# Kernel optimization log

Measured on AMD Instinct MI355X. Metric: run time of the kernel, lower is better.

The kernel has to match this reference:

```python
import jax, jax.numpy as jnp
import numpy as np

B, L, D, H, MLP = 8, 1024, 768, 12, 3072
DH = D // H
EPS = 1e-5


def setup_inputs() -> dict:
    key = jax.random.key(0)
    ks = jax.random.split(key, 8)
    s = 0.02
    return {
        "x": jax.random.normal(ks[0], (B, L, D), dtype=jnp.float32),
        "ln1_g": jnp.ones((D,), jnp.float32),
        "ln1_b": jnp.zeros((D,), jnp.float32),
        "w_qkv": jax.random.normal(ks[1], (3 * D, D), dtype=jnp.float32) * s,
        "w_out": jax.random.normal(ks[2], (D, D), dtype=jnp.float32) * s,
        "b_out": jnp.zeros((D,), jnp.float32),
        "ln2_g": jnp.ones((D,), jnp.float32),
        "ln2_b": jnp.zeros((D,), jnp.float32),
        "w1": jax.random.normal(ks[3], (MLP, D), dtype=jnp.float32) * s,
        "b1": jnp.zeros((MLP,), jnp.float32),
        "w2": jax.random.normal(ks[4], (D, MLP), dtype=jnp.float32) * s,
        "b2": jnp.zeros((D,), jnp.float32),
    }


def _layernorm(x, g, b):
    mu = jnp.mean(x, axis=-1, keepdims=True)
    var = jnp.mean(jnp.square(x - mu), axis=-1, keepdims=True)
    return (x - mu) * jax.lax.rsqrt(var + EPS) * g + b


def reference(x, ln1_g, ln1_b, w_qkv, w_out, b_out, ln2_g, ln2_b, w1, b1, w2, b2):
    # --- self-attention branch ---
    xn = _layernorm(x, ln1_g, ln1_b)                     # [B, L, D]
    qkv = jnp.einsum('bld,ed->ble', xn, w_qkv)           # [B, L, 3D]
    # rearrange 'b l (qkv h d) -> qkv b h l d'
    qkv = qkv.reshape(B, L, 3, H, DH).transpose(2, 0, 3, 1, 4)
    q, k, v = qkv[0], qkv[1], qkv[2]                     # [B, H, L, DH]
    scale = DH ** -0.5
    att = jnp.einsum('bhxd,bhyd->bhxy', q, k) * scale    # [B, H, L, L]
    att = jax.nn.softmax(att, axis=-1)
    o = jnp.einsum('bhxy,bhyd->bhxd', att, v)            # [B, H, L, DH]
    o = o.transpose(0, 2, 1, 3).reshape(B, L, D)         # 'b h l d -> b l (h d)'
    o = jnp.einsum('bld,ed->ble', o, w_out) + b_out
    x = x + o
    # --- MLP branch ---
    xn = _layernorm(x, ln2_g, ln2_b)
    h = jax.nn.gelu(jnp.einsum('bld,md->blm', xn, w1) + b1, approximate=False)
    h = jnp.einsum('blm,dm->bld', h, w2) + b2
    return x + h
```

## Files before the change

kernel.cpp:

```cpp
#include <hip/hip_runtime.h>
#include <hip/hip_bf16.h>
#include <math.h>

#define NB 8
#define NL 1024
#define ND 768
#define NH 12
#define NDH 64
#define NMLP 3072
#define NROWS 8192

typedef __attribute__((ext_vector_type(8))) short short8;
typedef __attribute__((ext_vector_type(8))) __bf16 bf16x8;
typedef __attribute__((ext_vector_type(4))) float f32x4;
typedef __attribute__((ext_vector_type(4))) float float4v;
typedef __attribute__((ext_vector_type(4))) unsigned short ushort4v;

__device__ __forceinline__ unsigned short f2b(float f) {
  unsigned u = __float_as_uint(f);
  unsigned r = (u + 0x7fffu + ((u >> 16) & 1u)) >> 16;
  return (unsigned short)r;
}

__device__ __forceinline__ f32x4 mfma16(short8 a, short8 b, f32x4 c) {
  return __builtin_amdgcn_mfma_f32_16x16x32_bf16(
      __builtin_bit_cast(bf16x8, a), __builtin_bit_cast(bf16x8, b), c, 0, 0, 0);
}

__device__ __forceinline__ void gl_lds16(const void* g, void* l) {
  __builtin_amdgcn_global_load_lds(
      (__attribute__((address_space(1))) void*)g,
      (__attribute__((address_space(3))) void*)l, 16, 0, 0);
}

__global__ __launch_bounds__(256) void cvt_all(const float* __restrict__ s0,
                                               const float* __restrict__ s1,
                                               const float* __restrict__ s2,
                                               const float* __restrict__ s3,
                                               unsigned short* __restrict__ d) {
  int i = (blockIdx.x * 256 + threadIdx.x) * 4;
  const float* s;
  int off;
  if (i < 1769472) { s = s0; off = i; }
  else if (i < 2359296) { s = s1; off = i - 1769472; }
  else if (i < 4718592) { s = s2; off = i - 2359296; }
  else { s = s3; off = i - 4718592; }
  float4v v = *(const float4v*)(s + off);
  ushort4v o;
  o[0] = f2b(v[0]); o[1] = f2b(v[1]); o[2] = f2b(v[2]); o[3] = f2b(v[3]);
  *(ushort4v*)(d + i) = o;
}

__global__ __launch_bounds__(256) void ln_bf16(const float* __restrict__ x,
                                               const float* __restrict__ g,
                                               const float* __restrict__ b,
                                               unsigned short* __restrict__ out) {
  int row = blockIdx.x, tid = threadIdx.x;
  const float* xr = x + (size_t)row * ND;
  float v0 = xr[tid], v1 = xr[tid + 256], v2 = xr[tid + 512];
  float s = v0 + v1 + v2;
  __shared__ float red[8];
#pragma unroll
  for (int o = 32; o > 0; o >>= 1) s += __shfl_down(s, o);
  int wv = tid >> 6, ln = tid & 63;
  if (ln == 0) red[wv] = s;
  __syncthreads();
  float mu = (red[0] + red[1] + red[2] + red[3]) * (1.0f / 768.0f);
  float d0 = v0 - mu, d1 = v1 - mu, d2 = v2 - mu;
  float q = d0 * d0 + d1 * d1 + d2 * d2;
#pragma unroll
  for (int o = 32; o > 0; o >>= 1) q += __shfl_down(q, o);
  if (ln == 0) red[4 + wv] = q;
  __syncthreads();
  float var = (red[4] + red[5] + red[6] + red[7]) * (1.0f / 768.0f);
  float rs = rsqrtf(var + 1e-5f);
  unsigned short* orow = out + (size_t)row * ND;
  orow[tid]       = f2b(d0 * rs * g[tid]       + b[tid]);
  orow[tid + 256] = f2b(d1 * rs * g[tid + 256] + b[tid + 256]);
  orow[tid + 512] = f2b(d2 * rs * g[tid + 512] + b[tid + 512]);
}

template <int MODE, int BM>
__global__ __launch_bounds__(256) void gemm_bt(
    const unsigned short* __restrict__ A, const unsigned short* __restrict__ W,
    unsigned short* __restrict__ outB, float* __restrict__ outF,
    const float* __restrict__ bias, const float* __restrict__ resid,
    int M, int N, int K, int gx) {
  constexpr int WN = (BM == 128) ? 2 : 4;
  constexpr int NJ = 128 / (WN * 16);
  constexpr int LDSA = BM * 32;
  __shared__ __attribute__((aligned(16))) unsigned short As[3 * LDSA];
  __shared__ __attribute__((aligned(16))) unsigned short Bs[3 * 4096];

  const int nwg = gridDim.x;
  const int bid = blockIdx.x;
  const int q = nwg >> 3, r = nwg & 7;
  const int xcd = bid & 7, idx = bid >> 3;
  const int swz = (xcd < r ? xcd * (q + 1) : r * (q + 1) + (xcd - r) * q) + idx;
  const int by = swz / gx, bx = swz - by * gx;
  const int m0 = by * BM, n0 = bx * 128;

  const int tid = threadIdx.x;
  const int wave = tid >> 6, lane = tid & 63;
  const int l15 = lane & 15, lhi = lane >> 4;
  const int wm = wave / WN, wn = wave % WN;

  const int sr = tid >> 2, sc8 = (tid & 3) * 8;
  const unsigned short* Ag0 = A + (size_t)(m0 + sr) * K + sc8;
  const unsigned short* Ag1 = Ag0 + (size_t)64 * K;
  const unsigned short* Wg0 = W + (size_t)(n0 + sr) * K + sc8;
  const unsigned short* Wg1 = Wg0 + (size_t)64 * K;

  f32x4 acc[4][NJ];
#pragma unroll
  for (int i = 0; i < 4; i++)
#pragma unroll
    for (int j = 0; j < NJ; j++) acc[i][j] = (f32x4){0.f, 0.f, 0.f, 0.f};

  auto STAGE = [&](int kelem, int buf) {
    unsigned short* Ad = As + buf * LDSA + wave * 512;
    unsigned short* Bd = Bs + buf * 4096 + wave * 512;
    gl_lds16(Ag0 + kelem, Ad);
    if constexpr (BM == 128) gl_lds16(Ag1 + kelem, Ad + 2048);
    gl_lds16(Wg0 + kelem, Bd);
    gl_lds16(Wg1 + kelem, Bd + 2048);
  };

  const int NT = K >> 5;
  STAGE(0, 0);
  STAGE(32, 1);

  int cb = 0, nbuf = 2;
  for (int t = 0; t < NT; ++t) {
    if (t + 2 < NT) {
      STAGE((t + 2) * 32, nbuf);
      if constexpr (BM == 128)
        asm volatile("s_waitcnt vmcnt(8)" ::: "memory");
      else
        asm volatile("s_waitcnt vmcnt(6)" ::: "memory");
    } else if (t + 2 == NT) {
      if constexpr (BM == 128)
        asm volatile("s_waitcnt vmcnt(4)" ::: "memory");
      else
        asm volatile("s_waitcnt vmcnt(3)" ::: "memory");
    } else {
      asm volatile("s_waitcnt vmcnt(0)" ::: "memory");
    }
    __builtin_amdgcn_s_barrier();

    const unsigned short* Ac = As + cb * LDSA;
    const unsigned short* Bc = Bs + cb * 4096;
    short8 af[4], bf[NJ];
#pragma unroll
    for (int i = 0; i < 4; i++)
      af[i] = *(const short8*)&Ac[(wm * 64 + i * 16 + l15) * 32 + lhi * 8];
#pragma unroll
    for (int j = 0; j < NJ; j++)
      bf[j] = *(const short8*)&Bc[(wn * (NJ * 16) + j * 16 + l15) * 32 + lhi * 8];
#pragma unroll
    for (int i = 0; i < 4; i++)
#pragma unroll
      for (int j = 0; j < NJ; j++) acc[i][j] = mfma16(af[i], bf[j], acc[i][j]);

    asm volatile("s_waitcnt lgkmcnt(0)" ::: "memory");
    __builtin_amdgcn_s_barrier();
    cb = (cb == 2) ? 0 : cb + 1;
    nbuf = (nbuf == 2) ? 0 : nbuf + 1;
  }

#pragma unroll
  for (int i = 0; i < 4; i++) {
    int row = m0 + wm * 64 + i * 16 + lhi * 4;
#pragma unroll
    for (int j = 0; j < NJ; j++) {
      int col = n0 + wn * (NJ * 16) + j * 16 + l15;
#pragma unroll
      for (int r2 = 0; r2 < 4; r2++) {
        float v = acc[i][j][r2];
        size_t idxo = (size_t)(row + r2) * N + col;
        if (MODE == 0) {
          outB[idxo] = f2b(v);
        } else if (MODE == 2) {
          float t2 = v + bias[col];
          float z = 1.5957691f * t2 * (1.0f + 0.044715f * t2 * t2);
          float e = __expf(-z);
          outB[idxo] = f2b(__fdividef(t2, 1.0f + e));
        } else {
          outF[idxo] = v + bias[col] + resid[idxo];
        }
      }
    }
  }
}

__global__ __launch_bounds__(256) void vtrans(const unsigned short* __restrict__ qkv,
                                              unsigned short* __restrict__ vT) {
  int bid = blockIdx.x;
  int tt = bid & 15;
  int t2 = bid >> 4;
  int h = t2 % NH, b = t2 / NH;
  __shared__ unsigned short L[64 * 72];
  int t = threadIdx.x;
  int row0 = t >> 3;
  int col8 = (t & 7) * 8;
#pragma unroll
  for (int s = 0; s < 2; s++) {
    int row = row0 + s * 32;
    const unsigned short* src =
        qkv + ((size_t)(b * NL + tt * 64 + row)) * 2304 + 1536 + h * 64 + col8;
    short8 v = *(const short8*)src;
    int wchunk = row >> 3;
#pragma unroll
    for (int j = 0; j < 8; j++) {
      int d = col8 + j;
      int cp = wchunk ^ (d >> 3);
      L[d * 72 + cp * 8 + (row & 7)] = (unsigned short)v[j];
    }
  }
  __syncthreads();
#pragma unroll
  for (int s = 0; s < 2; s++) {
    int d = (t >> 3) + s * 32;
    int rc = t & 7;
    int cp = rc ^ (d >> 3);
    short8 ov = *(const short8*)&L[d * 72 + cp * 8];
    *(short8*)(vT + ((size_t)((b * NH + h) * 64 + d)) * NL + tt * 64 + rc * 8) = ov;
  }
}

__global__ __launch_bounds__(256, 3) void attn_kernel(
    const unsigned short* __restrict__ qkv, const unsigned short* __restrict__ vT,
    unsigned short* __restrict__ o) {
  int bid = blockIdx.x;
  int qt = bid & 7;
  int t = bid >> 3;
  int h = t % NH, b = t / NH;
  const int tid = threadIdx.x;
  const int wave = tid >> 6, lane = tid & 63;
  const int l15 = lane & 15, lhi = lane >> 4;
  const int sw = l15 & 7;
  __shared__ __attribute__((aligned(16))) unsigned short Ks[2 * 64 * 64];
  __shared__ __attribute__((aligned(16))) unsigned short Vs[2 * 64 * 64];
  __shared__ __attribute__((aligned(16))) unsigned short Ps[4 * 16 * 64];

  const unsigned short* qp = qkv + (size_t)(b * NL + qt * 128) * 2304 + h * 64;
  short8 qf[2][2];
#pragma unroll
  for (int i = 0; i < 2; i++)
#pragma unroll
    for (int kk = 0; kk < 2; kk++)
      qf[i][kk] = *(const short8*)(qp + (size_t)(i * 64 + wave * 16 + l15) * 2304 +
                                   kk * 32 + lhi * 8);

  const int srow = tid >> 3, scpos = tid & 7;
  const int sc8 = (scpos ^ (srow & 7)) * 8;
  const unsigned short* ks0 =
      qkv + (size_t)(b * NL + srow) * 2304 + 768 + h * 64 + sc8;
  const unsigned short* vt0 =
      vT + (size_t)((b * NH + h) * 64 + srow) * NL + sc8;
  unsigned short* Pw = Ps + wave * 1024;

  float mrow[2][4];
  f32x4 acc[2][4];
  f32x4 accL[2];
#pragma unroll
  for (int i = 0; i < 2; i++) {
#pragma unroll
    for (int r = 0; r < 4; r++) mrow[i][r] = -1e30f;
    accL[i] = (f32x4){0.f, 0.f, 0.f, 0.f};
#pragma unroll
    for (int nb = 0; nb < 4; nb++) acc[i][nb] = (f32x4){0.f, 0.f, 0.f, 0.f};
  }

  short8 onesf;
#pragma unroll
  for (int j = 0; j < 8; j++) onesf[j] = (short)0x3F80;

#define STAGE(ktile, buf)                                                    \
  {                                                                          \
    const unsigned short* ksrc = ks0 + (size_t)((ktile) * 64) * 2304;        \
    const unsigned short* vsrc = vt0 + (ktile) * 64;                         \
    unsigned short* kb_ = Ks + (buf) * 4096 + wave * 512;                    \
    unsigned short* vb_ = Vs + (buf) * 4096 + wave * 512;                    \
    gl_lds16(ksrc, kb_);                                                     \
    gl_lds16(ksrc + (size_t)32 * 2304, kb_ + 2048);                          \
    gl_lds16(vsrc, vb_);                                                     \
    gl_lds16(vsrc + 32 * NL, vb_ + 2048);                                    \
  }

  STAGE(0, 0);

  for (int kt = 0; kt < 16; kt++) {
    const int cb = kt & 1;
    if (kt + 1 < 16) {
      STAGE(kt + 1, cb ^ 1);
      asm volatile("s_waitcnt vmcnt(4)" ::: "memory");
    } else {
      asm volatile("s_waitcnt vmcnt(0)" ::: "memory");
    }
    __builtin_amdgcn_s_barrier();

    const unsigned short* Kc = Ks + cb * 4096;
    const unsigned short* Vc = Vs + cb * 4096;

    short8 vf[4][2];
#pragma unroll
    for (int nb = 0; nb < 4; nb++)
#pragma unroll
      for (int kk = 0; kk < 2; kk++)
        vf[nb][kk] =
            *(const short8*)&Vc[(nb * 16 + l15) * 64 + ((kk * 4 + lhi) ^ sw) * 8];

#pragma unroll
    for (int i = 0; i < 2; i++) {
      f32x4 sv[4];
#pragma unroll
      for (int kb = 0; kb < 4; kb++) {
        short8 kf0 = *(const short8*)&Kc[(kb * 16 + l15) * 64 + (lhi ^ sw) * 8];
        short8 kf1 = *(const short8*)&Kc[(kb * 16 + l15) * 64 + ((4 + lhi) ^ sw) * 8];
        f32x4 s = mfma16(qf[i][0], kf0, (f32x4){0.f, 0.f, 0.f, 0.f});
        sv[kb] = mfma16(qf[i][1], kf1, s);
      }
      float xmax[4];
#pragma unroll
      for (int r = 0; r < 4; r++) {
        float x = fmaxf(fmaxf(sv[0][r], sv[1][r]), fmaxf(sv[2][r], sv[3][r]));
#pragma unroll
        for (int m = 1; m < 16; m <<= 1) x = fmaxf(x, __shfl_xor(x, m));
        xmax[r] = x;
      }
      bool ok = (xmax[0] <= mrow[i][0] + 64.f) & (xmax[1] <= mrow[i][1] + 64.f) &
                (xmax[2] <= mrow[i][2] + 64.f) & (xmax[3] <= mrow[i][3] + 64.f);
      if (!__all(ok)) {
#pragma unroll
        for (int r = 0; r < 4; r++) {
          float mnew = fmaxf(mrow[i][r], xmax[r]);
          float corr = __expf((mrow[i][r] - mnew) * 0.125f);
          mrow[i][r] = mnew;
#pragma unroll
          for (int nb = 0; nb < 4; nb++) acc[i][nb][r] *= corr;
          accL[i][r] *= corr;
        }
      }
      float mm[4];
#pragma unroll
      for (int r = 0; r < 4; r++) mm[r] = -mrow[i][r] * 0.125f;
#pragma unroll
      for (int kb = 0; kb < 4; kb++) {
        int ch = kb * 2 + (l15 >> 3);
#pragma unroll
        for (int r = 0; r < 4; r++) {
          int row = lhi * 4 + r;
          float p = __expf(fmaf(sv[kb][r], 0.125f, mm[r]));
          unsigned short pu =
              (unsigned short)((__float_as_uint(p) + 0x8000u) >> 16);
          Pw[row * 64 + ((ch ^ (row & 7)) << 3) + sw] = pu;
        }
      }
      short8 pf0 = *(const short8*)&Pw[l15 * 64 + (lhi ^ sw) * 8];
      short8 pf1 = *(const short8*)&Pw[l15 * 64 + ((4 + lhi) ^ sw) * 8];
#pragma unroll
      for (int nb = 0; nb < 4; nb++) {
        acc[i][nb] = mfma16(pf0, vf[nb][0], acc[i][nb]);
        acc[i][nb] = mfma16(pf1, vf[nb][1], acc[i][nb]);
      }
      accL[i] = mfma16(pf0, onesf, accL[i]);
      accL[i] = mfma16(pf1, onesf, accL[i]);
    }
    __builtin_amdgcn_s_barrier();
  }
#undef STAGE

#pragma unroll
  for (int i = 0; i < 2; i++) {
    float inv[4];
#pragma unroll
    for (int r = 0; r < 4; r++) inv[r] = 1.0f / accL[i][r];
    size_t obase =
        (size_t)(b * NL + qt * 128 + i * 64 + wave * 16 + lhi * 4) * ND + h * 64;
#pragma unroll
    for (int nb = 0; nb < 4; nb++)
#pragma unroll
      for (int r = 0; r < 4; r++)
        o[obase + (size_t)r * ND + nb * 16 + l15] = f2b(acc[i][nb][r] * inv[r]);
  }
}

extern "C" void kernel_launch(void* const* d_in, const int* in_sizes, int n_in,
                              void* d_out, int out_size, void* d_ws, size_t ws_size,
                              hipStream_t stream) {
  const float* x     = (const float*)d_in[0];
  const float* ln1_g = (const float*)d_in[1];
  const float* ln1_b = (const float*)d_in[2];
  const float* w_qkv = (const float*)d_in[3];
  const float* w_out = (const float*)d_in[4];
  const float* b_out = (const float*)d_in[5];
  const float* ln2_g = (const float*)d_in[6];
  const float* ln2_b = (const float*)d_in[7];
  const float* w1    = (const float*)d_in[8];
  const float* b1    = (const float*)d_in[9];
  const float* w2    = (const float*)d_in[10];
  const float* b2    = (const float*)d_in[11];
  float* out = (float*)d_out;

  char* p = (char*)d_ws;
  unsigned short* wqkv_b = (unsigned short*)p; p += (size_t)2304 * 768 * 2;
  unsigned short* wout_b = (unsigned short*)p; p += (size_t)768 * 768 * 2;
  unsigned short* w1_b   = (unsigned short*)p; p += (size_t)3072 * 768 * 2;
  unsigned short* w2_b   = (unsigned short*)p; p += (size_t)768 * 3072 * 2;
  unsigned short* xn     = (unsigned short*)p; p += (size_t)NROWS * ND * 2;
  unsigned short* qkvb   = (unsigned short*)p; p += (size_t)NROWS * NMLP * 2;
  float* x1 = (float*)p;  p += (size_t)NROWS * ND * 4;
  unsigned short* vTb = (unsigned short*)x1;

  cvt_all<<<7077888 / 4 / 256, 256, 0, stream>>>(w_qkv, w_out, w1, w2, wqkv_b);

  ln_bf16<<<NROWS, 256, 0, stream>>>(x, ln1_g, ln1_b, xn);
  gemm_bt<0, 128><<<1152, 256, 0, stream>>>(
      xn, wqkv_b, qkvb, nullptr, nullptr, nullptr, NROWS, 2304, 768, 18);
  vtrans<<<NB * NH * (NL / 64), 256, 0, stream>>>(qkvb, vTb);
  attn_kernel<<<NB * NH * (NL / 128), 256, 0, stream>>>(qkvb, vTb, xn);
  gemm_bt<1, 64><<<768, 256, 0, stream>>>(
      xn, wout_b, nullptr, x1, b_out, x, NROWS, 768, 768, 6);
  ln_bf16<<<NROWS, 256, 0, stream>>>(x1, ln2_g, ln2_b, xn);
  gemm_bt<2, 128><<<1536, 256, 0, stream>>>(
      xn, w1_b, qkvb, nullptr, b1, nullptr, NROWS, 3072, 768, 24);
  gemm_bt<3, 64><<<768, 256, 0, stream>>>(
      qkvb, w2_b, nullptr, out, b2, x1, NROWS, 768, 3072, 6);
}
```

Measured before the change: 296.0 us.

## Add dedicated 64-row GEMM kernel with K=64 tiles and swizzled LDS

Splits the GEMM template so the two N=768 GEMMs (out-projection and MLP down-projection) use a new 64x128 kernel. It stages K=64 per step with double buffering and an XOR-swizzled LDS layout meant to avoid bank conflicts. Each wave now covers all 64 rows by 32 columns. The intent is fewer barriers per K step and better LDS read efficiency on these narrow-output GEMMs. In exchange it uses more LDS per block and keeps one fewer buffer in flight than the triple-buffered version.

```diff
diff --git a/kernel.cpp b/kernel.cpp
--- a/kernel.cpp
+++ b/kernel.cpp
@@ -80,16 +80,12 @@
   orow[tid + 512] = f2b(d2 * rs * g[tid + 512] + b[tid + 512]);
 }
 
-template <int MODE, int BM>
+template <int MODE>
 __global__ __launch_bounds__(256) void gemm_bt(
     const unsigned short* __restrict__ A, const unsigned short* __restrict__ W,
-    unsigned short* __restrict__ outB, float* __restrict__ outF,
-    const float* __restrict__ bias, const float* __restrict__ resid,
+    unsigned short* __restrict__ outB, const float* __restrict__ bias,
     int M, int N, int K, int gx) {
-  constexpr int WN = (BM == 128) ? 2 : 4;
-  constexpr int NJ = 128 / (WN * 16);
-  constexpr int LDSA = BM * 32;
-  __shared__ __attribute__((aligned(16))) unsigned short As[3 * LDSA];
+  __shared__ __attribute__((aligned(16))) unsigned short As[3 * 4096];
   __shared__ __attribute__((aligned(16))) unsigned short Bs[3 * 4096];
 
   const int nwg = gridDim.x;
@@ -98,12 +94,12 @@
   const int xcd = bid & 7, idx = bid >> 3;
   const int swz = (xcd < r ? xcd * (q + 1) : r * (q + 1) + (xcd - r) * q) + idx;
   const int by = swz / gx, bx = swz - by * gx;
-  const int m0 = by * BM, n0 = bx * 128;
+  const int m0 = by * 128, n0 = bx * 128;
 
   const int tid = threadIdx.x;
   const int wave = tid >> 6, lane = tid & 63;
   const int l15 = lane & 15, lhi = lane >> 4;
-  const int wm = wave / WN, wn = wave % WN;
+  const int wm = wave >> 1, wn = wave & 1;
 
   const int sr = tid >> 2, sc8 = (tid & 3) * 8;
   const unsigned short* Ag0 = A + (size_t)(m0 + sr) * K + sc8;
@@ -111,17 +107,17 @@
   const unsigned short* Wg0 = W + (size_t)(n0 + sr) * K + sc8;
   const unsigned short* Wg1 = Wg0 + (size_t)64 * K;
 
-  f32x4 acc[4][NJ];
+  f32x4 acc[4][4];
 #pragma unroll
   for (int i = 0; i < 4; i++)
 #pragma unroll
-    for (int j = 0; j < NJ; j++) acc[i][j] = (f32x4){0.f, 0.f, 0.f, 0.f};
+    for (int j = 0; j < 4; j++) acc[i][j] = (f32x4){0.f, 0.f, 0.f, 0.f};
 
   auto STAGE = [&](int kelem, int buf) {
-    unsigned short* Ad = As + buf * LDSA + wave * 512;
+    unsigned short* Ad = As + buf * 4096 + wave * 512;
     unsigned short* Bd = Bs + buf * 4096 + wave * 512;
     gl_lds16(Ag0 + kelem, Ad);
-    if constexpr (BM == 128) gl_lds16(Ag1 + kelem, Ad + 2048);
+    gl_lds16(Ag1 + kelem, Ad + 2048);
     gl_lds16(Wg0 + kelem, Bd);
     gl_lds16(Wg1 + kelem, Bd + 2048);
   };
@@ -134,33 +130,27 @@
   for (int t = 0; t < NT; ++t) {
     if (t + 2 < NT) {
       STAGE((t + 2) * 32, nbuf);
-      if constexpr (BM == 128)
-        asm volatile("s_waitcnt vmcnt(8)" ::: "memory");
-      else
-        asm volatile("s_waitcnt vmcnt(6)" ::: "memory");
+      asm volatile("s_waitcnt vmcnt(8)" ::: "memory");
     } else if (t + 2 == NT) {
-      if constexpr (BM == 128)
-        asm volatile("s_waitcnt vmcnt(4)" ::: "memory");
-      else
-        asm volatile("s_waitcnt vmcnt(3)" ::: "memory");
+      asm volatile("s_waitcnt vmcnt(4)" ::: "memory");
     } else {
       asm volatile("s_waitcnt vmcnt(0)" ::: "memory");
     }
     __builtin_amdgcn_s_barrier();
 
-    const unsigned short* Ac = As + cb * LDSA;
+    const unsigned short* Ac = As + cb * 4096;
     const unsigned short* Bc = Bs + cb * 4096;
-    short8 af[4], bf[NJ];
+    short8 af[4], bf[4];
 #pragma unroll
     for (int i = 0; i < 4; i++)
       af[i] = *(const short8*)&Ac[(wm * 64 + i * 16 + l15) * 32 + lhi * 8];
 #pragma unroll
-    for (int j = 0; j < NJ; j++)
-      bf[j] = *(const short8*)&Bc[(wn * (NJ * 16) + j * 16 + l15) * 32 + lhi * 8];
+    for (int j = 0; j < 4; j++)
+      bf[j] = *(const short8*)&Bc[(wn * 64 + j * 16 + l15) * 32 + lhi * 8];
 #pragma unroll
     for (int i = 0; i < 4; i++)
 #pragma unroll
-      for (int j = 0; j < NJ; j++) acc[i][j] = mfma16(af[i], bf[j], acc[i][j]);
+      for (int j = 0; j < 4; j++) acc[i][j] = mfma16(af[i], bf[j], acc[i][j]);
 
     asm volatile("s_waitcnt lgkmcnt(0)" ::: "memory");
     __builtin_amdgcn_s_barrier();
@@ -172,22 +162,120 @@
   for (int i = 0; i < 4; i++) {
     int row = m0 + wm * 64 + i * 16 + lhi * 4;
 #pragma unroll
-    for (int j = 0; j < NJ; j++) {
-      int col = n0 + wn * (NJ * 16) + j * 16 + l15;
+    for (int j = 0; j < 4; j++) {
+      int col = n0 + wn * 64 + j * 16 + l15;
 #pragma unroll
       for (int r2 = 0; r2 < 4; r2++) {
         float v = acc[i][j][r2];
         size_t idxo = (size_t)(row + r2) * N + col;
         if (MODE == 0) {
           outB[idxo] = f2b(v);
-        } else if (MODE == 2) {
+        } else {
           float t2 = v + bias[col];
           float z = 1.5957691f * t2 * (1.0f + 0.044715f * t2 * t2);
           float e = __expf(-z);
           outB[idxo] = f2b(__fdividef(t2, 1.0f + e));
-        } else {
-          outF[idxo] = v + bias[col] + resid[idxo];
         }
+      }
+    }
+  }
+}
+
+template <int MODE>
+__global__ __launch_bounds__(256) void gemm_bt64(
+    const unsigned short* __restrict__ A, const unsigned short* __restrict__ W,
+    float* __restrict__ outF, const float* __restrict__ bias,
+    const float* __restrict__ resid, int M, int N, int K, int gx) {
+  __shared__ __attribute__((aligned(16))) unsigned short As[2 * 4096];
+  __shared__ __attribute__((aligned(16))) unsigned short Bs[2 * 8192];
+
+  const int nwg = gridDim.x;
+  const int bid = blockIdx.x;
+  const int q = nwg >> 3, r = nwg & 7;
+  const int xcd = bid & 7, idx = bid >> 3;
+  const int swz = (xcd < r ? xcd * (q + 1) : r * (q + 1) + (xcd - r) * q) + idx;
+  const int by = swz / gx, bx = swz - by * gx;
+  const int m0 = by * 64, n0 = bx * 128;
+
+  const int tid = threadIdx.x;
+  const int wave = tid >> 6, lane = tid & 63;
+  const int l15 = lane & 15, lhi = lane >> 4;
+  const int wn = wave;
+
+  const int sr = tid >> 3;
+  const int swc8 = ((tid & 7) ^ (sr & 7)) * 8;
+  const unsigned short* Aga = A + (size_t)(m0 + sr) * K + swc8;
+  const unsigned short* Wga = W + (size_t)(n0 + sr) * K + swc8;
+
+  f32x4 acc[4][2];
+#pragma unroll
+  for (int i = 0; i < 4; i++)
+#pragma unroll
+    for (int j = 0; j < 2; j++) acc[i][j] = (f32x4){0.f, 0.f, 0.f, 0.f};
+
+  auto STAGE = [&](int kelem, int buf) {
+    unsigned short* Ad = As + buf * 4096 + wave * 512;
+    unsigned short* Bd = Bs + buf * 8192 + wave * 512;
+    gl_lds16(Aga + kelem, Ad);
+    gl_lds16(Aga + (size_t)32 * K + kelem, Ad + 2048);
+    gl_lds16(Wga + kelem, Bd);
+    gl_lds16(Wga + (size_t)32 * K + kelem, Bd + 2048);
+    gl_lds16(Wga + (size_t)64 * K + kelem, Bd + 4096);
+    gl_lds16(Wga + (size_t)96 * K + kelem, Bd + 6144);
+  };
+
+  const int NT = K >> 6;
+  STAGE(0, 0);
+
+  for (int t = 0; t < NT; ++t) {
+    const int cb = t & 1;
+    if (t + 1 < NT) {
+      STAGE((t + 1) * 64, cb ^ 1);
+      asm volatile("s_waitcnt vmcnt(6)" ::: "memory");
+    } else {
+      asm volatile("s_waitcnt vmcnt(0)" ::: "memory");
+    }
+    __builtin_amdgcn_s_barrier();
+
+    const unsigned short* Ac = As + cb * 4096;
+    const unsigned short* Bc = Bs + cb * 8192;
+    short8 af[4][2], bf[2][2];
+#pragma unroll
+    for (int i = 0; i < 4; i++) {
+      int ar = i * 16 + l15;
+#pragma unroll
+      for (int kk = 0; kk < 2; kk++)
+        af[i][kk] = *(const short8*)&Ac[ar * 64 + (((kk * 4 + lhi) ^ (ar & 7)) * 8)];
+    }
+#pragma unroll
+    for (int j = 0; j < 2; j++) {
+      int br = wn * 32 + j * 16 + l15;
+#pragma unroll
+      for (int kk = 0; kk < 2; kk++)
+        bf[j][kk] = *(const short8*)&Bc[br * 64 + (((kk * 4 + lhi) ^ (br & 7)) * 8)];
+    }
+#pragma unroll
+    for (int kk = 0; kk < 2; kk++)
+#pragma unroll
+      for (int i = 0; i < 4; i++)
+#pragma unroll
+        for (int j = 0; j < 2; j++)
+          acc[i][j] = mfma16(af[i][kk], bf[j][kk], acc[i][j]);
+
+    asm volatile("s_waitcnt lgkmcnt(0)" ::: "memory");
+    __builtin_amdgcn_s_barrier();
+  }
+
+#pragma unroll
+  for (int i = 0; i < 4; i++) {
+    int row = m0 + i * 16 + lhi * 4;
+#pragma unroll
+    for (int j = 0; j < 2; j++) {
+      int col = n0 + wn * 32 + j * 16 + l15;
+#pragma unroll
+      for (int r2 = 0; r2 < 4; r2++) {
+        size_t idxo = (size_t)(row + r2) * N + col;
+        outF[idxo] = acc[i][j][r2] + bias[col] + resid[idxo];
       }
     }
   }
@@ -416,15 +504,15 @@
   cvt_all<<<7077888 / 4 / 256, 256, 0, stream>>>(w_qkv, w_out, w1, w2, wqkv_b);
 
   ln_bf16<<<NROWS, 256, 0, stream>>>(x, ln1_g, ln1_b, xn);
-  gemm_bt<0, 128><<<1152, 256, 0, stream>>>(
-      xn, wqkv_b, qkvb, nullptr, nullptr, nullptr, NROWS, 2304, 768, 18);
+  gemm_bt<0><<<1152, 256, 0, stream>>>(
+      xn, wqkv_b, qkvb, nullptr, NROWS, 2304, 768, 18);
   vtrans<<<NB * NH * (NL / 64), 256, 0, stream>>>(qkvb, vTb);
   attn_kernel<<<NB * NH * (NL / 128), 256, 0, stream>>>(qkvb, vTb, xn);
-  gemm_bt<1, 64><<<768, 256, 0, stream>>>(
-      xn, wout_b, nullptr, x1, b_out, x, NROWS, 768, 768, 6);
+  gemm_bt64<1><<<768, 256, 0, stream>>>(
+      xn, wout_b, x1, b_out, x, NROWS, 768, 768, 6);
   ln_bf16<<<NROWS, 256, 0, stream>>>(x1, ln2_g, ln2_b, xn);
-  gemm_bt<2, 128><<<1536, 256, 0, stream>>>(
-      xn, w1_b, qkvb, nullptr, b1, nullptr, NROWS, 3072, 768, 24);
-  gemm_bt<3, 64><<<768, 256, 0, stream>>>(
-      qkvb, w2_b, nullptr, out, b2, x1, NROWS, 768, 3072, 6);
-}
+  gemm_bt<2><<<1536, 256, 0, stream>>>(
+      xn, w1_b, qkvb, b1, NROWS, 3072, 768, 24);
+  gemm_bt64<3><<<768, 256, 0, stream>>>(
+      qkvb, w2_b, out, b2, x1, NROWS, 768, 3072, 6);
+}
```

After: 273.1 us. 1.08x faster.
